# Kernel optimization log

Hardware: AMD Instinct MI355X
Metric: run time of the kernel (lower is better)

## Reference

```python
import jax, jax.numpy as jnp
import numpy as np

NEMB = 512
NEMBDIM = 64
NHIDDEN = 1024
NINPUT = 784
COMMIT_COST = 0.25


def setup_inputs() -> dict:
    key = jax.random.key(0)
    ks = jax.random.split(key, 16)
    B = 32768
    x = jax.random.uniform(ks[0], (B, NINPUT), dtype=jnp.float32)
    # codebook: uniform(-1/nemb, 1/nemb) as in torch init
    emb = jax.random.uniform(ks[1], (NEMB, NEMBDIM), dtype=jnp.float32,
                             minval=-1.0 / NEMB, maxval=1.0 / NEMB)
    s = 0.02
    We1 = jax.random.normal(ks[2], (NHIDDEN, NINPUT), dtype=jnp.float32) * s
    be1 = jnp.zeros((NHIDDEN,), jnp.float32)
    We2 = jax.random.normal(ks[3], (NHIDDEN, NHIDDEN), dtype=jnp.float32) * s
    be2 = jnp.zeros((NHIDDEN,), jnp.float32)
    We3 = jax.random.normal(ks[4], (NEMBDIM, NHIDDEN), dtype=jnp.float32) * s
    be3 = jnp.zeros((NEMBDIM,), jnp.float32)
    Wd1 = jax.random.normal(ks[5], (NHIDDEN, NEMBDIM), dtype=jnp.float32) * s
    bd1 = jnp.zeros((NHIDDEN,), jnp.float32)
    Wd2 = jax.random.normal(ks[6], (NHIDDEN, NHIDDEN), dtype=jnp.float32) * s
    bd2 = jnp.zeros((NHIDDEN,), jnp.float32)
    Wd3 = jax.random.normal(ks[7], (NINPUT, NHIDDEN), dtype=jnp.float32) * s
    bd3 = jnp.zeros((NINPUT,), jnp.float32)
    return dict(x=x, emb=emb, We1=We1, be1=be1, We2=We2, be2=be2, We3=We3, be3=be3,
                Wd1=Wd1, bd1=bd1, Wd2=Wd2, bd2=bd2, Wd3=Wd3, bd3=bd3)


def reference(x, emb, We1, be1, We2, be2, We3, be3, Wd1, bd1, Wd2, bd2, Wd3, bd3):
    # Encoder MLP (dropout inactive at inference)
    h = jax.nn.relu(x @ We1.T + be1)
    h = jax.nn.relu(h @ We2.T + be2)
    z = h @ We3.T + be3  # [B, nembdim]

    # VQ codebook lookup. NOTE: original code omits the factor 2 on the cross
    # term (sum(z^2) + sum(e^2) - z @ e.T); we reproduce it faithfully.
    d = (jnp.sum(z * z, axis=1, keepdims=True)
         + jnp.sum(emb * emb, axis=1)
         - z @ emb.T)  # [B, nemb]
    idx = jnp.argmin(d, axis=1)  # [B]
    q = emb[idx]  # gather == one-hot @ emb, same math

    code_loss = jnp.mean((q - jax.lax.stop_gradient(z)) ** 2)
    commit_loss = jnp.mean((jax.lax.stop_gradient(q) - z) ** 2)
    loss = code_loss + COMMIT_COST * commit_loss

    # straight-through estimator
    q_st = z + jax.lax.stop_gradient(q - z)

    # Decoder MLP
    h = jax.nn.relu(q_st @ Wd1.T + bd1)
    h = jax.nn.relu(h @ Wd2.T + bd2)
    out = jax.nn.sigmoid(h @ Wd3.T + bd3)
    return out, loss
```

## Files before the change

kernel.cpp:

```cpp
#include <hip/hip_runtime.h>
#include <stdint.h>
#include <stddef.h>

typedef __bf16 bf16x8 __attribute__((ext_vector_type(8)));
typedef float  f32x4  __attribute__((ext_vector_type(4)));
typedef float  f32x16 __attribute__((ext_vector_type(16)));
typedef int    i32x8  __attribute__((ext_vector_type(8)));
typedef unsigned short u16;
typedef unsigned char  u8;

#define NIN   784
#define NINP  896
#define NH    1024
#define NE    512
#define ND    64
#define NOUTP 1024

#define BAR()   asm volatile("s_barrier" ::: "memory")
#define LGKM0() asm volatile("s_waitcnt lgkmcnt(0)" ::: "memory")
#define VM4()   asm volatile("s_waitcnt vmcnt(4)" ::: "memory")
#define VM3()   asm volatile("s_waitcnt vmcnt(3)" ::: "memory")
#define VM0()   asm volatile("s_waitcnt vmcnt(0)" ::: "memory")
#define FSWZ(r) (((r) ^ ((r) >> 2)) & 3)
#define SCL1    0x7F7F7F7F
#define GLDS(g, l) __builtin_amdgcn_global_load_lds((__attribute__((address_space(1))) void*)(g), (__attribute__((address_space(3))) void*)(l), 16, 0, 0)

static __device__ __forceinline__ u16 f2bf(float f) {
  union { float f; unsigned u; } v; v.f = f;
  unsigned r = v.u + 0x7fffu + ((v.u >> 16) & 1u);
  return (u16)(r >> 16);
}
static __device__ __forceinline__ float bf2f(u16 b) {
  union { unsigned u; float f; } v; v.u = ((unsigned)b) << 16; return v.f;
}
static __device__ __forceinline__ unsigned pack4fp8(float a, float b, float c, float d) {
  unsigned p;
  asm("v_cvt_pk_fp8_f32 %0, %1, %2" : "=v"(p) : "v"(a), "v"(b));
  asm("v_cvt_pk_fp8_f32 %0, %1, %2 op_sel:[0,0,1]" : "+v"(p) : "v"(c), "v"(d));
  return p;
}
static __device__ __forceinline__ u8 f2fp8(float a) {
  unsigned p;
  asm("v_cvt_pk_fp8_f32 %0, %1, %2" : "=v"(p) : "v"(a), "v"(a));
  return (u8)(p & 0xff);
}


__global__ void cast_tiled8(const float* __restrict__ src, u8* __restrict__ dst,
                            int R, int C, int Cp) {
  int r = blockIdx.y;
  int c4 = (blockIdx.x * blockDim.x + threadIdx.x) * 4;
  if (c4 >= Cp) return;
  unsigned o = 0;
  if (r < R && c4 < C) {
    const float4 v = *(const float4*)&src[(size_t)r * C + c4];
    o = pack4fp8(v.x, v.y, v.z, v.w);
  }
  size_t off = ((size_t)(r >> 8) * (Cp >> 6) + (c4 >> 6)) * 16384
             + ((r & 255) << 6) + ((((c4 >> 4) & 3) ^ FSWZ(r)) << 4) + (c4 & 15);
  *(unsigned*)&dst[off] = o;
}

__global__ void cast_rm8(const float* __restrict__ src, u8* __restrict__ dst, int R, int C) {
  int r = blockIdx.y;
  int c4 = (blockIdx.x * blockDim.x + threadIdx.x) * 4;
  if (c4 >= C) return;
  const float4 v = *(const float4*)&src[(size_t)r * C + c4];
  *(unsigned*)&dst[(size_t)r * C + c4] = pack4fp8(v.x, v.y, v.z, v.w);
}

__global__ void emb_prep(const float* __restrict__ emb, u16* __restrict__ ebf,
                         float* __restrict__ cvec) {
  int j = blockIdx.x, l = threadIdx.x;
  float v = emb[j * ND + l];
  ebf[j * 64 + (((l >> 3) ^ (j & 7)) << 3) + (l & 7)] = f2bf(v);
  float s = v * v;
  #pragma unroll
  for (int off = 32; off > 0; off >>= 1) s += __shfl_down(s, off);
  if (l == 0) cvec[j] = s;
}

template <int ACT, int OMODE, bool NCHK>
__global__ __launch_bounds__(256, 3)
void gemm128mx(const u8* __restrict__ A, const u8* __restrict__ Bm,
               const float* __restrict__ bias, float* __restrict__ Cf,
               u8* __restrict__ Cb, int N, int K, int ldc, int ntiles) {
  __shared__ __attribute__((aligned(128))) u8 lds[32768];
  const int tid = threadIdx.x, lane = tid & 63, w = tid >> 6;
  const int wr = w >> 1, wc = w & 1;
  const int l31 = lane & 31, h = lane >> 5;

  int nwg = gridDim.x, cpx = nwg >> 3, b = blockIdx.x;
  int sb = (b & 7) * cpx + (b >> 3);
  int tm = sb / ntiles, tn = sb % ntiles;

  const int NT = K >> 6;
  const u8* Ap = A + (size_t)(tm >> 1) * NT * 16384 + (size_t)(tm & 1) * 8192;
  const u8* Bp = Bm + (size_t)(tn >> 1) * NT * 16384 + (size_t)(tn & 1) * 8192;

  auto stage = [&](int t, int buf) {
    #pragma unroll
    for (int i = 0; i < 2; ++i)
      GLDS(Ap + (size_t)t * 16384 + ((i * 256 + tid) << 4),
           lds + buf * 8192 + ((i * 256 + w * 64) << 4));
    #pragma unroll
    for (int i = 0; i < 2; ++i)
      GLDS(Bp + (size_t)t * 16384 + ((i * 256 + tid) << 4),
           lds + 16384 + buf * 8192 + ((i * 256 + w * 64) << 4));
  };

  f32x16 acc[2][2] = {};
  stage(0, 0);
  if (NT > 1) stage(1, 1);

  for (int t = 0; t < NT; ++t) {
    const int buf = t & 1;
    if (t + 1 < NT) { VM4(); } else { VM0(); }
    BAR();
    const u8* lA = lds + buf * 8192;
    const u8* lB = lds + 16384 + buf * 8192;
    i32x8 af[2], bf_[2];
    #pragma unroll
    for (int s = 0; s < 2; ++s) {
      int row = wr * 64 + s * 32 + l31;
      int F = FSWZ(row);
      const u8* base = lA + row * 64;
      int4 lo = *(const int4*)&base[(((h << 1)    ) ^ F) << 4];
      int4 hi = *(const int4*)&base[(((h << 1) | 1) ^ F) << 4];
      af[s][0] = lo.x; af[s][1] = lo.y; af[s][2] = lo.z; af[s][3] = lo.w;
      af[s][4] = hi.x; af[s][5] = hi.y; af[s][6] = hi.z; af[s][7] = hi.w;
    }
    #pragma unroll
    for (int s = 0; s < 2; ++s) {
      int row = wc * 64 + s * 32 + l31;
      int F = FSWZ(row);
      const u8* base = lB + row * 64;
      int4 lo = *(const int4*)&base[(((h << 1)    ) ^ F) << 4];
      int4 hi = *(const int4*)&base[(((h << 1) | 1) ^ F) << 4];
      bf_[s][0] = lo.x; bf_[s][1] = lo.y; bf_[s][2] = lo.z; bf_[s][3] = lo.w;
      bf_[s][4] = hi.x; bf_[s][5] = hi.y; bf_[s][6] = hi.z; bf_[s][7] = hi.w;
    }
    LGKM0();
    BAR();
    if (t + 2 < NT) stage(t + 2, buf);
    #pragma unroll
    for (int ms = 0; ms < 2; ++ms)
      #pragma unroll
      for (int ns = 0; ns < 2; ++ns)
        acc[ms][ns] = __builtin_amdgcn_mfma_scale_f32_32x32x64_f8f6f4(
            af[ms], bf_[ns], acc[ms][ns], 0, 0, 0, SCL1, 0, SCL1);
  }

  float bv[2];
  #pragma unroll
  for (int ns = 0; ns < 2; ++ns) {
    int col = tn * 128 + wc * 64 + ns * 32 + l31;
    bv[ns] = (!NCHK || col < N) ? bias[col] : 0.f;
  }

  if (OMODE == 0) {
    #pragma unroll
    for (int ms = 0; ms < 2; ++ms)
      #pragma unroll
      for (int r = 0; r < 16; ++r) {
        int row = tm * 128 + wr * 64 + ms * 32 + (r & 3) + ((r >> 2) << 3) + (h << 2);
        #pragma unroll
        for (int ns = 0; ns < 2; ++ns) {
          int col = tn * 128 + wc * 64 + ns * 32 + l31;
          if (NCHK && col >= N) continue;
          float v = acc[ms][ns][r] + bv[ns];
          if (ACT == 1) v = fmaxf(v, 0.f);
          if (ACT == 2) v = 1.f / (1.f + __expf(-v));
          Cf[(size_t)row * ldc + col] = v;
        }
      }
  } else {
    float* lf = (float*)lds;
    #pragma unroll
    for (int p = 0; p < 2; ++p) {
      __syncthreads();
      if (wr == p) {
        #pragma unroll
        for (int ms = 0; ms < 2; ++ms)
          #pragma unroll
          for (int r = 0; r < 16; ++r) {
            int lrow = ms * 32 + (r & 3) + ((r >> 2) << 3) + (h << 2);
            #pragma unroll
            for (int ns = 0; ns < 2; ++ns) {
              int col = wc * 64 + ns * 32 + l31;
              float v = acc[ms][ns][r] + bv[ns];
              if (ACT == 1) v = fmaxf(v, 0.f);
              lf[lrow * 128 + (((col >> 2) ^ (lrow & 31)) << 2) + (col & 3)] = v;
            }
          }
      }
      __syncthreads();
      #pragma unroll
      for (int it = 0; it < 2; ++it) {
        int idx = it * 256 + tid;
        int lrow = idx >> 3, cc = idx & 7;
        f32x4 q[4];
        #pragma unroll
        for (int s = 0; s < 4; ++s)
          q[s] = *(const f32x4*)&lf[lrow * 128 + (((cc * 4 + s) ^ (lrow & 31)) << 2)];
        int R = tm * 128 + p * 64 + lrow;
        int C = tn * 128 + cc * 16;
        int4 o;
        o.x = pack4fp8(q[0][0], q[0][1], q[0][2], q[0][3]);
        o.y = pack4fp8(q[1][0], q[1][1], q[1][2], q[1][3]);
        o.z = pack4fp8(q[2][0], q[2][1], q[2][2], q[2][3]);
        o.w = pack4fp8(q[3][0], q[3][1], q[3][2], q[3][3]);
        size_t off = ((size_t)(R >> 8) * (ldc >> 6) + (C >> 6)) * 16384
                   + ((R & 255) << 6) + ((((C >> 4) & 3) ^ FSWZ(R)) << 4);
        *(int4*)&Cb[off] = o;
      }
    }
  }
}

__global__ __launch_bounds__(256, 1)
void z_vq(const u8* __restrict__ Atiled,
          const u8* __restrict__ Wrm,
          const float* __restrict__ be3,
          const u16* __restrict__ ebf,
          const float* __restrict__ cvec,
          u8* __restrict__ qb8, float* __restrict__ lossacc) {
  __shared__ u8 lsA[2][128 * 64];
  __shared__ u8 lsW[2][64 * 64];
  __shared__ u16 embl[512 * 64];
  __shared__ float zls[128 * 68];
  __shared__ int bidxl[128];

  const int t = threadIdx.x;
  const int lane = t & 63;
  const int w = t >> 6;
  const int lr = lane & 15, hi = lane >> 4;
  const int tm = blockIdx.x;

  #pragma unroll
  for (int i = 0; i < 16; ++i) {
    const u16* g = ebf + (size_t)((i * 256 + t) << 3);
    u16* l = embl + (size_t)((i * 256 + w * 64) << 3);
    GLDS(g, l);
  }

  const size_t abase0 = ((size_t)(tm >> 1) * 16) * 16384 + (size_t)(tm & 1) * 8192;
  auto stageA = [&](int kt, int buf) {
    #pragma unroll
    for (int i = 0; i < 2; ++i) {
      const u8* g = Atiled + abase0 + (size_t)kt * 16384 + ((i * 256 + t) << 4);
      u8* l = lsA[buf] + ((i * 256 + w * 64) << 4);
      GLDS(g, l);
    }
  };
  auto stageW = [&](int kt, int buf) {
    int row = w * 16 + (lane >> 2), p = lane & 3;
    const u8* g = Wrm + (size_t)row * 1024 + kt * 64 + ((p ^ FSWZ(row)) << 4);
    u8* l = lsW[buf] + ((w * 64) << 4);
    GLDS(g, l);
  };

  f32x4 acc[2][4] = {};
  stageA(0, 0); stageW(0, 0);
  stageA(1, 1); stageW(1, 1);
  for (int kt = 0; kt < 16; ++kt) {
    const int bf = kt & 1;
    if (kt < 15) { VM3(); } else { VM0(); }
    BAR();
    #pragma unroll
    for (int kk = 0; kk < 64; kk += 32) {
      long af[2], bfr[4];
      #pragma unroll
      for (int m = 0; m < 2; ++m) {
        int row = w * 32 + m * 16 + lr;
        int ch = ((kk >> 4) + (hi >> 1)) ^ FSWZ(row);
        af[m] = *(const long*)&lsA[bf][row * 64 + ch * 16 + ((hi & 1) << 3)];
      }
      #pragma unroll
      for (int n = 0; n < 4; ++n) {
        int row = n * 16 + lr;
        int ch = ((kk >> 4) + (hi >> 1)) ^ FSWZ(row);
        bfr[n] = *(const long*)&lsW[bf][row * 64 + ch * 16 + ((hi & 1) << 3)];
      }
      #pragma unroll
      for (int m = 0; m < 2; ++m)
        #pragma unroll
        for (int n = 0; n < 4; ++n)
          acc[m][n] = __builtin_amdgcn_mfma_f32_16x16x32_fp8_fp8(af[m], bfr[n], acc[m][n], 0, 0, 0);
    }
    LGKM0();
    BAR();
    if (kt + 2 < 16) { stageA(kt + 2, bf); stageW(kt + 2, bf); }
  }

  #pragma unroll
  for (int m = 0; m < 2; ++m)
    #pragma unroll
    for (int j = 0; j < 4; ++j) {
      int row = w * 32 + m * 16 + hi * 4 + j;
      #pragma unroll
      for (int n = 0; n < 4; ++n) {
        int col = n * 16 + lr;
        zls[row * 68 + col] = acc[m][n][j] + be3[col];
      }
    }
  __syncthreads();

  bf16x8 azf[2][2];
  #pragma unroll
  for (int rt = 0; rt < 2; ++rt)
    #pragma unroll
    for (int kf = 0; kf < 2; ++kf) {
      int row = w * 32 + rt * 16 + lr;
      union { bf16x8 v; u16 u[8]; } pk;
      #pragma unroll
      for (int e = 0; e < 8; ++e)
        pk.u[e] = f2bf(zls[row * 68 + kf * 32 + hi * 8 + e]);
      azf[rt][kf] = pk.v;
    }

  float bvv[2][4]; int bii[2][4];
  #pragma unroll
  for (int rt = 0; rt < 2; ++rt)
    #pragma unroll
    for (int j = 0; j < 4; ++j) { bvv[rt][j] = 3.4e38f; bii[rt][j] = 0; }

  for (int ct = 0; ct < 32; ++ct) {
    bf16x8 bqf[2];
    #pragma unroll
    for (int kf = 0; kf < 2; ++kf) {
      int row = ct * 16 + lr;
      int ch = (kf * 4 + hi) ^ (row & 7);
      bqf[kf] = *(const bf16x8*)&embl[row * 64 + ch * 8];
    }
    float cv = cvec[ct * 16 + lr];
    #pragma unroll
    for (int rt = 0; rt < 2; ++rt) {
      f32x4 sc = {};
      sc = __builtin_amdgcn_mfma_f32_16x16x32_bf16(azf[rt][0], bqf[0], sc, 0, 0, 0);
      sc = __builtin_amdgcn_mfma_f32_16x16x32_bf16(azf[rt][1], bqf[1], sc, 0, 0, 0);
      int code = ct * 16 + lr;
      #pragma unroll
      for (int j = 0; j < 4; ++j) {
        float d = cv - sc[j];
        if (d < bvv[rt][j]) { bvv[rt][j] = d; bii[rt][j] = code; }
      }
    }
  }
  #pragma unroll
  for (int off = 1; off < 16; off <<= 1) {
    #pragma unroll
    for (int rt = 0; rt < 2; ++rt)
      #pragma unroll
      for (int j = 0; j < 4; ++j) {
        float ov = __shfl_xor(bvv[rt][j], off);
        int   oi = __shfl_xor(bii[rt][j], off);
        if (ov < bvv[rt][j] || (ov == bvv[rt][j] && oi < bii[rt][j])) {
          bvv[rt][j] = ov; bii[rt][j] = oi;
        }
      }
  }
  if (lr == 0) {
    #pragma unroll
    for (int rt = 0; rt < 2; ++rt)
      #pragma unroll
      for (int j = 0; j < 4; ++j)
        bidxl[w * 32 + rt * 16 + hi * 4 + j] = bii[rt][j];
  }
  __syncthreads();

  const int gr0 = tm * 128;
  float ls = 0.f;
  #pragma unroll 4
  for (int r8 = 0; r8 < 32; ++r8) {
    int row = w * 32 + r8;
    int bi = bidxl[row];
    u16 qu = embl[bi * 64 + (((lane >> 3) ^ (bi & 7)) << 3) + (lane & 7)];
    float qf = bf2f(qu);
    float d = qf - zls[row * 68 + lane];
    ls += d * d;
    int R = gr0 + row;
    qb8[(size_t)R * 64 + ((((lane >> 4) & 3) ^ FSWZ(R)) << 4) + (lane & 15)] = f2fp8(qf);
  }
  #pragma unroll
  for (int off = 32; off > 0; off >>= 1) ls += __shfl_down(ls, off);
  if (lane == 0) atomicAdd(lossacc, ls);
}

__global__ void loss_final(const float* __restrict__ acc, float* __restrict__ o, float denom) {
  o[0] = acc[0] * 1.25f / denom;
}

extern "C" void kernel_launch(void* const* d_in, const int* in_sizes, int n_in,
                              void* d_out, int out_size, void* d_ws, size_t ws_size,
                              hipStream_t stream) {
  const float* x   = (const float*)d_in[0];
  const float* emb = (const float*)d_in[1];
  const float* We1 = (const float*)d_in[2];
  const float* be1 = (const float*)d_in[3];
  const float* We2 = (const float*)d_in[4];
  const float* be2 = (const float*)d_in[5];
  const float* We3 = (const float*)d_in[6];
  const float* be3 = (const float*)d_in[7];
  const float* Wd1 = (const float*)d_in[8];
  const float* bd1 = (const float*)d_in[9];
  const float* Wd2 = (const float*)d_in[10];
  const float* bd2 = (const float*)d_in[11];
  const float* Wd3 = (const float*)d_in[12];
  const float* bd3 = (const float*)d_in[13];

  const int Bn = in_sizes[0] / NIN;
  float* out = (float*)d_out;
  float* out_loss = out + (size_t)Bn * NIN;

  char* ws = (char*)d_ws;
  size_t off = 0;
  auto take = [&](size_t bytes) { char* p = ws + off; off += (bytes + 255) & ~(size_t)255; return p; };

  u8*    xpad8 = (u8*)take((size_t)Bn * NINP);
  u8*    hA8   = (u8*)take((size_t)Bn * NH);
  u8*    hB8   = (u8*)take((size_t)Bn * NH);
  u8*    qb8   = (u8*)take((size_t)Bn * ND);
  u8*    we1p8 = (u8*)take((size_t)NH * NINP);
  u8*    we2b8 = (u8*)take((size_t)NH * NH);
  u8*    we3r8 = (u8*)take((size_t)64 * NH);
  u8*    wd1b8 = (u8*)take((size_t)NH * ND);
  u8*    wd2b8 = (u8*)take((size_t)NH * NH);
  u8*    wd3p8 = (u8*)take((size_t)NOUTP * NH);
  u16*   embb  = (u16*)take((size_t)NE * ND * 2);
  float* cvec  = (float*)take(NE * 4);
  float* lossa = (float*)take(4);

  hipMemsetAsync(lossa, 0, 4, stream);

  cast_tiled8<<<dim3(1, Bn),    256, 0, stream>>>(x,   xpad8, Bn,  NIN, NINP);
  cast_tiled8<<<dim3(1, NH),    256, 0, stream>>>(We1, we1p8, NH,  NIN, NINP);
  cast_tiled8<<<dim3(1, NH),    256, 0, stream>>>(We2, we2b8, NH,  NH,  NH);
  cast_rm8   <<<dim3(1, 64),    256, 0, stream>>>(We3, we3r8, 64,  NH);
  cast_tiled8<<<dim3(1, NH),    256, 0, stream>>>(Wd1, wd1b8, NH,  ND,  ND);
  cast_tiled8<<<dim3(1, NH),    256, 0, stream>>>(Wd2, wd2b8, NH,  NH,  NH);
  cast_tiled8<<<dim3(1, NOUTP), 256, 0, stream>>>(Wd3, wd3p8, NIN, NH,  NH);
  emb_prep<<<NE, 64, 0, stream>>>(emb, embb, cvec);

  const int mt = Bn / 128;
  gemm128mx<1,1,false><<<mt * 8, 256, 0, stream>>>(xpad8, we1p8, be1, nullptr, hA8, NH, NINP, NH, 8);
  gemm128mx<1,1,false><<<mt * 8, 256, 0, stream>>>(hA8, we2b8, be2, nullptr, hB8, NH, NH, NH, 8);
  z_vq<<<Bn / 128, 256, 0, stream>>>(hB8, we3r8, be3, embb, cvec, qb8, lossa);
  gemm128mx<1,1,false><<<mt * 8, 256, 0, stream>>>(qb8, wd1b8, bd1, nullptr, hA8, NH, 64, NH, 8);
  gemm128mx<1,1,false><<<mt * 8, 256, 0, stream>>>(hA8, wd2b8, bd2, nullptr, hB8, NH, NH, NH, 8);
  gemm128mx<2,0,true ><<<mt * 7, 256, 0, stream>>>(hB8, wd3p8, bd3, out, nullptr, NIN, NH, NIN, 7);

  loss_final<<<1, 1, 0, stream>>>(lossa, out_loss, (float)Bn * ND);
}
```

Baseline: 264.6 us.

## Triple-buffer GEMM pipelines, trim K padding, merge weight prep and loss launches

The GEMM and z_vq main loops move from double to triple LDS buffering with deeper vmcnt waits, so more global loads are in flight ahead of compute. Input padding on the first layer shrinks from 896 to 832 columns, cutting K-tiles and x-cast traffic. The six weight casts merge into one launch. The memset and final-loss kernel are replaced by an in-kernel zeroing step and a last-block ticket, which removes several small launches. In exchange, GEMM LDS use grows to 48KB per block, which may cap occupancy at 3 blocks per CU.

```diff
diff --git a/kernel.cpp b/kernel.cpp
--- a/kernel.cpp
+++ b/kernel.cpp
@@ -10,7 +10,7 @@
 typedef unsigned char  u8;
 
 #define NIN   784
-#define NINP  896
+#define NINP  832
 #define NH    1024
 #define NE    512
 #define ND    64
@@ -18,6 +18,8 @@
 
 #define BAR()   asm volatile("s_barrier" ::: "memory")
 #define LGKM0() asm volatile("s_waitcnt lgkmcnt(0)" ::: "memory")
+#define VM8()   asm volatile("s_waitcnt vmcnt(8)" ::: "memory")
+#define VM6()   asm volatile("s_waitcnt vmcnt(6)" ::: "memory")
 #define VM4()   asm volatile("s_waitcnt vmcnt(4)" ::: "memory")
 #define VM3()   asm volatile("s_waitcnt vmcnt(3)" ::: "memory")
 #define VM0()   asm volatile("s_waitcnt vmcnt(0)" ::: "memory")
@@ -45,6 +47,10 @@
   return (u8)(p & 0xff);
 }
 
+static __device__ __forceinline__ size_t t8off(int r, int c, int Cp) {
+  return ((size_t)(r >> 8) * (Cp >> 6) + (c >> 6)) * 16384
+       + ((r & 255) << 6) + ((((c >> 4) & 3) ^ FSWZ(r)) << 4) + (c & 15);
+}
 
 __global__ void cast_tiled8(const float* __restrict__ src, u8* __restrict__ dst,
                             int R, int C, int Cp) {
@@ -56,22 +62,40 @@
     const float4 v = *(const float4*)&src[(size_t)r * C + c4];
     o = pack4fp8(v.x, v.y, v.z, v.w);
   }
-  size_t off = ((size_t)(r >> 8) * (Cp >> 6) + (c4 >> 6)) * 16384
-             + ((r & 255) << 6) + ((((c4 >> 4) & 3) ^ FSWZ(r)) << 4) + (c4 & 15);
-  *(unsigned*)&dst[off] = o;
-}
-
-__global__ void cast_rm8(const float* __restrict__ src, u8* __restrict__ dst, int R, int C) {
-  int r = blockIdx.y;
-  int c4 = (blockIdx.x * blockDim.x + threadIdx.x) * 4;
-  if (c4 >= C) return;
-  const float4 v = *(const float4*)&src[(size_t)r * C + c4];
-  *(unsigned*)&dst[(size_t)r * C + c4] = pack4fp8(v.x, v.y, v.z, v.w);
+  *(unsigned*)&dst[t8off(r, c4, Cp)] = o;
+}
+
+__global__ void prep_weights(const float* __restrict__ We1, const float* __restrict__ We2,
+                             const float* __restrict__ Wd1, const float* __restrict__ Wd2,
+                             const float* __restrict__ Wd3, const float* __restrict__ We3,
+                             u8* __restrict__ d0, u8* __restrict__ d1, u8* __restrict__ d2,
+                             u8* __restrict__ d3, u8* __restrict__ d4, u8* __restrict__ d5) {
+  int id = blockIdx.z, r = blockIdx.y;
+  int c4 = threadIdx.x * 4;
+  const float* src; u8* dst; int R, C, Cp; bool rm = false;
+  switch (id) {
+    case 0: src = We1; dst = d0; R = 1024; C = NIN;  Cp = NINP; break;
+    case 1: src = We2; dst = d1; R = 1024; C = 1024; Cp = 1024; break;
+    case 2: src = Wd1; dst = d2; R = 1024; C = 64;   Cp = 64;   break;
+    case 3: src = Wd2; dst = d3; R = 1024; C = 1024; Cp = 1024; break;
+    case 4: src = Wd3; dst = d4; R = NIN;  C = 1024; Cp = 1024; break;
+    default: src = We3; dst = d5; R = 64;  C = 1024; Cp = 1024; rm = true; break;
+  }
+  if (c4 >= Cp || (rm && r >= R)) return;
+  unsigned o = 0;
+  if (r < R && c4 < C) {
+    const float4 v = *(const float4*)&src[(size_t)r * C + c4];
+    o = pack4fp8(v.x, v.y, v.z, v.w);
+  }
+  if (rm) *(unsigned*)&dst[(size_t)r * Cp + c4] = o;
+  else    *(unsigned*)&dst[t8off(r, c4, Cp)] = o;
 }
 
 __global__ void emb_prep(const float* __restrict__ emb, u16* __restrict__ ebf,
-                         float* __restrict__ cvec) {
+                         float* __restrict__ cvec, float* __restrict__ lossa,
+                         unsigned* __restrict__ tick) {
   int j = blockIdx.x, l = threadIdx.x;
+  if (j == 0 && l == 0) { lossa[0] = 0.f; tick[0] = 0u; }
   float v = emb[j * ND + l];
   ebf[j * 64 + (((l >> 3) ^ (j & 7)) << 3) + (l & 7)] = f2bf(v);
   float s = v * v;
@@ -85,7 +109,7 @@
 void gemm128mx(const u8* __restrict__ A, const u8* __restrict__ Bm,
                const float* __restrict__ bias, float* __restrict__ Cf,
                u8* __restrict__ Cb, int N, int K, int ldc, int ntiles) {
-  __shared__ __attribute__((aligned(128))) u8 lds[32768];
+  __shared__ __attribute__((aligned(128))) u8 lds[49152];
   const int tid = threadIdx.x, lane = tid & 63, w = tid >> 6;
   const int wr = w >> 1, wc = w & 1;
   const int l31 = lane & 31, h = lane >> 5;
@@ -106,19 +130,20 @@
     #pragma unroll
     for (int i = 0; i < 2; ++i)
       GLDS(Bp + (size_t)t * 16384 + ((i * 256 + tid) << 4),
-           lds + 16384 + buf * 8192 + ((i * 256 + w * 64) << 4));
+           lds + 24576 + buf * 8192 + ((i * 256 + w * 64) << 4));
   };
 
   f32x16 acc[2][2] = {};
   stage(0, 0);
   if (NT > 1) stage(1, 1);
+  if (NT > 2) stage(2, 2);
 
   for (int t = 0; t < NT; ++t) {
-    const int buf = t & 1;
-    if (t + 1 < NT) { VM4(); } else { VM0(); }
+    const int buf = t % 3;
+    if (t + 2 < NT) { VM8(); } else if (t + 1 < NT) { VM4(); } else { VM0(); }
     BAR();
     const u8* lA = lds + buf * 8192;
-    const u8* lB = lds + 16384 + buf * 8192;
+    const u8* lB = lds + 24576 + buf * 8192;
     i32x8 af[2], bf_[2];
     #pragma unroll
     for (int s = 0; s < 2; ++s) {
@@ -142,7 +167,7 @@
     }
     LGKM0();
     BAR();
-    if (t + 2 < NT) stage(t + 2, buf);
+    if (t + 3 < NT) stage(t + 3, buf);
     #pragma unroll
     for (int ms = 0; ms < 2; ++ms)
       #pragma unroll
@@ -210,23 +235,20 @@
         o.y = pack4fp8(q[1][0], q[1][1], q[1][2], q[1][3]);
         o.z = pack4fp8(q[2][0], q[2][1], q[2][2], q[2][3]);
         o.w = pack4fp8(q[3][0], q[3][1], q[3][2], q[3][3]);
-        size_t off = ((size_t)(R >> 8) * (ldc >> 6) + (C >> 6)) * 16384
-                   + ((R & 255) << 6) + ((((C >> 4) & 3) ^ FSWZ(R)) << 4);
-        *(int4*)&Cb[off] = o;
+        *(int4*)&Cb[t8off(R, C, ldc)] = o;
       }
     }
   }
 }
 
 __global__ __launch_bounds__(256, 1)
-void z_vq(const u8* __restrict__ Atiled,
-          const u8* __restrict__ Wrm,
-          const float* __restrict__ be3,
-          const u16* __restrict__ ebf,
-          const float* __restrict__ cvec,
-          u8* __restrict__ qb8, float* __restrict__ lossacc) {
-  __shared__ u8 lsA[2][128 * 64];
-  __shared__ u8 lsW[2][64 * 64];
+void z_vq(const u8* __restrict__ Atiled, const u8* __restrict__ Wrm,
+          const float* __restrict__ be3, const u16* __restrict__ ebf,
+          const float* __restrict__ cvec, u8* __restrict__ qb8,
+          float* __restrict__ lossacc, unsigned* __restrict__ tick,
+          float* __restrict__ out_loss, float denom) {
+  __shared__ u8 lsA[3][128 * 64];
+  __shared__ u8 lsW[3][64 * 64];
   __shared__ u16 embl[512 * 64];
   __shared__ float zls[128 * 68];
   __shared__ int bidxl[128];
@@ -263,9 +285,10 @@
   f32x4 acc[2][4] = {};
   stageA(0, 0); stageW(0, 0);
   stageA(1, 1); stageW(1, 1);
+  stageA(2, 2); stageW(2, 2);
   for (int kt = 0; kt < 16; ++kt) {
-    const int bf = kt & 1;
-    if (kt < 15) { VM3(); } else { VM0(); }
+    const int bf = kt % 3;
+    if (kt < 14) { VM6(); } else if (kt == 14) { VM3(); } else { VM0(); }
     BAR();
     #pragma unroll
     for (int kk = 0; kk < 64; kk += 32) {
@@ -290,7 +313,7 @@
     }
     LGKM0();
     BAR();
-    if (kt + 2 < 16) { stageA(kt + 2, bf); stageW(kt + 2, bf); }
+    if (kt + 3 < 16) { stageA(kt + 3, bf); stageW(kt + 3, bf); }
   }
 
   #pragma unroll
@@ -385,10 +408,16 @@
   #pragma unroll
   for (int off = 32; off > 0; off >>= 1) ls += __shfl_down(ls, off);
   if (lane == 0) atomicAdd(lossacc, ls);
-}
-
-__global__ void loss_final(const float* __restrict__ acc, float* __restrict__ o, float denom) {
-  o[0] = acc[0] * 1.25f / denom;
+
+  __syncthreads();
+  if (t == 0) {
+    __threadfence();
+    unsigned tk = atomicAdd(tick, 1u);
+    if (tk == gridDim.x - 1) {
+      float v = atomicAdd(lossacc, 0.f);
+      out_loss[0] = v * 1.25f / denom;
+    }
+  }
 }
 
 extern "C" void kernel_launch(void* const* d_in, const int* in_sizes, int n_in,
@@ -430,25 +459,19 @@
   u16*   embb  = (u16*)take((size_t)NE * ND * 2);
   float* cvec  = (float*)take(NE * 4);
   float* lossa = (float*)take(4);
-
-  hipMemsetAsync(lossa, 0, 4, stream);
-
-  cast_tiled8<<<dim3(1, Bn),    256, 0, stream>>>(x,   xpad8, Bn,  NIN, NINP);
-  cast_tiled8<<<dim3(1, NH),    256, 0, stream>>>(We1, we1p8, NH,  NIN, NINP);
-  cast_tiled8<<<dim3(1, NH),    256, 0, stream>>>(We2, we2b8, NH,  NH,  NH);
-  cast_rm8   <<<dim3(1, 64),    256, 0, stream>>>(We3, we3r8, 64,  NH);
-  cast_tiled8<<<dim3(1, NH),    256, 0, stream>>>(Wd1, wd1b8, NH,  ND,  ND);
-  cast_tiled8<<<dim3(1, NH),    256, 0, stream>>>(Wd2, wd2b8, NH,  NH,  NH);
-  cast_tiled8<<<dim3(1, NOUTP), 256, 0, stream>>>(Wd3, wd3p8, NIN, NH,  NH);
-  emb_prep<<<NE, 64, 0, stream>>>(emb, embb, cvec);
+  unsigned* tick = (unsigned*)take(4);
+
+  cast_tiled8<<<dim3(1, Bn), 256, 0, stream>>>(x, xpad8, Bn, NIN, NINP);
+  prep_weights<<<dim3(1, 1024, 6), 256, 0, stream>>>(We1, We2, Wd1, Wd2, Wd3, We3,
+                                                     we1p8, we2b8, wd1b8, wd2b8, wd3p8, we3r8);
+  emb_prep<<<NE, 64, 0, stream>>>(emb, embb, cvec, lossa, tick);
 
   const int mt = Bn / 128;
   gemm128mx<1,1,false><<<mt * 8, 256, 0, stream>>>(xpad8, we1p8, be1, nullptr, hA8, NH, NINP, NH, 8);
   gemm128mx<1,1,false><<<mt * 8, 256, 0, stream>>>(hA8, we2b8, be2, nullptr, hB8, NH, NH, NH, 8);
-  z_vq<<<Bn / 128, 256, 0, stream>>>(hB8, we3r8, be3, embb, cvec, qb8, lossa);
+  z_vq<<<Bn / 128, 256, 0, stream>>>(hB8, we3r8, be3, embb, cvec, qb8, lossa, tick,
+                                     out_loss, (float)Bn * ND);
   gemm128mx<1,1,false><<<mt * 8, 256, 0, stream>>>(qb8, wd1b8, bd1, nullptr, hA8, NH, 64, NH, 8);
   gemm128mx<1,1,false><<<mt * 8, 256, 0, stream>>>(hA8, wd2b8, bd2, nullptr, hB8, NH, NH, NH, 8);
   gemm128mx<2,0,true ><<<mt * 7, 256, 0, stream>>>(hB8, wd3p8, bd3, out, nullptr, NIN, NH, NIN, 7);
-
-  loss_final<<<1, 1, 0, stream>>>(lossa, out_loss, (float)Bn * ND);
-}
+}
```

New measurement: 277.1 us. 1.05x slower.
